# Kernel tuning notes

Hardware: AMD Instinct MI355X
Metric: run time of the kernel (lower is better)

The kernel has to match this reference:

```python
import jax, jax.numpy as jnp
import numpy as np

B, MAX_T, S, H, NB, NA = 64, 511, 1024, 4096, 8, 4


def setup_inputs() -> dict:
    key = jax.random.key(0)
    k1, k2, k3, k4, k5 = jax.random.split(key, 5)
    s_i_batch = jax.random.normal(k1, (B, MAX_T + 1, S), dtype=jnp.float32)
    actions_batch = jax.random.randint(k2, (B, MAX_T), 0, NA, dtype=jnp.int32)
    lengths = jax.random.randint(k3, (B,), 0, MAX_T, dtype=jnp.int32)
    W1 = jax.random.normal(k4, (S, H), dtype=jnp.float32) * (1.0 / np.sqrt(S))
    b1 = jnp.zeros((H,), dtype=jnp.float32)
    W2 = jax.random.normal(k5, (H, NB * NA), dtype=jnp.float32) * (1.0 / np.sqrt(H))
    b2 = jnp.zeros((NB * NA,), dtype=jnp.float32)
    return {"s_i_batch": s_i_batch, "actions_batch": actions_batch,
            "lengths": lengths, "W1": W1, "b1": b1, "W2": W2, "b2": b2}


def reference(s_i_batch, actions_batch, lengths, W1, b1, W2, b2):
    Bc, Tp1, _ = s_i_batch.shape
    maxT = Tp1 - 1
    # control_net: MLP -> per-(option, action) log-probs
    h = jax.nn.relu(jnp.einsum('bts,sh->bth', s_i_batch, W1) + b1)
    logits = (jnp.einsum('bth,ha->bta', h, W2) + b2).reshape(Bc, Tp1, NB, NA)
    action_logps = jax.nn.log_softmax(logits, axis=-1)  # (B, T+1, b, 4)
    # option 0, timesteps 0..max_T-1
    lp0 = action_logps[:, :maxT, 0, :]                  # (B, max_T, 4)
    gathered = jnp.take_along_axis(lp0, actions_batch[..., None].astype(jnp.int32), axis=-1)[..., 0]
    mask = (jnp.arange(maxT)[None, :] < lengths[:, None]).astype(lp0.dtype)  # (B, max_T)
    total_logp = jnp.sum(gathered * mask)
    return -total_logp
```

## Files before the change

kernel.cpp:

```cpp
#include <hip/hip_runtime.h>
#include <hip/hip_bf16.h>
#include <math.h>

#define B_    64
#define MAXT  511
#define TP1   512
#define S_    1024
#define H_    4096
#define M_TOTAL (B_*TP1)
#define NITER (S_/32)

typedef __attribute__((ext_vector_type(8))) short  short8;
typedef __attribute__((ext_vector_type(4))) float  float4v;

#define ZBUF_BYTES (M_TOTAL*4*sizeof(float))
#define ACC_OFF    ZBUF_BYTES
#define SBF_OFF    0x81000
#define SBF_BYTES  ((size_t)M_TOTAL*S_*2)
#define W1T_OFF    (SBF_OFF + SBF_BYTES)

static __device__ __forceinline__ unsigned short f2bf(float f) {
    unsigned int u = __float_as_uint(f);
    u = u + 0x7fffu + ((u >> 16) & 1u);
    return (unsigned short)(u >> 16);
}

__global__ __launch_bounds__(128) void cvt_s_kernel(const float* __restrict__ s,
                                                    const int* __restrict__ lengths,
                                                    unsigned short* __restrict__ out) {
    int row = blockIdx.x;
    int b = row >> 9, t = row & 511;
    if (t >= lengths[b]) return;
    size_t idx = (size_t)row * S_ + threadIdx.x * 8;
    float4v f0 = *(const float4v*)(s + idx);
    float4v f1 = *(const float4v*)(s + idx + 4);
    short8 o;
    o[0] = (short)f2bf(f0[0]); o[1] = (short)f2bf(f0[1]);
    o[2] = (short)f2bf(f0[2]); o[3] = (short)f2bf(f0[3]);
    o[4] = (short)f2bf(f1[0]); o[5] = (short)f2bf(f1[1]);
    o[6] = (short)f2bf(f1[2]); o[7] = (short)f2bf(f1[3]);
    *(short8*)(out + idx) = o;
}

__global__ void cvt_w1t_kernel(const float* __restrict__ W1, unsigned short* __restrict__ W1T) {
    __shared__ float tile[32][33];
    int h0 = blockIdx.x * 32;
    int k0 = blockIdx.y * 32;
    int tx = threadIdx.x & 31, ty = threadIdx.x >> 5;
    for (int r = ty; r < 32; r += 8)
        tile[r][tx] = W1[(size_t)(k0 + r) * H_ + h0 + tx];
    __syncthreads();
    for (int r = ty; r < 32; r += 8)
        W1T[(size_t)(h0 + r) * S_ + k0 + tx] = f2bf(tile[tx][r]);
}

__global__ __launch_bounds__(256) void gemm_fused_kernel(
        const unsigned short* __restrict__ Sb,
        const unsigned short* __restrict__ W1T,
        const float* __restrict__ b1,
        const float* __restrict__ W2,
        const int*   __restrict__ lengths,
        float*       __restrict__ zbuf)
{
    int ntile = blockIdx.x;
    int mtile = blockIdx.y;
    int b  = mtile >> 2;
    int t0 = (mtile & 3) * 128;
    if (lengths[b] <= t0) return;

    int m0 = mtile * 128;
    int n0 = ntile * 128;

    __shared__ unsigned short smemA[2 * 128 * 32];
    __shared__ unsigned short smemB[2 * 128 * 32];

    int tid  = threadIdx.x;
    int wid  = tid >> 6;
    int lane = tid & 63;
    int lane15 = lane & 15;
    int quad   = lane >> 4;
    int wave_m = (wid >> 1) * 64;
    int wave_n = (wid & 1) * 64;

    int cA0 = tid, cA1 = tid + 256;
    int mA0 = cA0 >> 2, cp0 = cA0 & 3, q0 = cp0 ^ ((mA0 >> 1) & 3);
    int mA1 = cA1 >> 2, cp1 = cA1 & 3, q1 = cp1 ^ ((mA1 >> 1) & 3);

    const char* gA0 = (const char*)Sb  + (size_t)(m0 + mA0) * (S_*2) + q0 * 16;
    const char* gA1 = (const char*)Sb  + (size_t)(m0 + mA1) * (S_*2) + q1 * 16;
    const char* gB0 = (const char*)W1T + (size_t)(n0 + mA0) * (S_*2) + q0 * 16;
    const char* gB1 = (const char*)W1T + (size_t)(n0 + mA1) * (S_*2) + q1 * 16;
    char* lwA0 = (char*)smemA + cA0 * 16;
    char* lwA1 = (char*)smemA + cA1 * 16;
    char* lwB0 = (char*)smemB + cA0 * 16;
    char* lwB1 = (char*)smemB + cA1 * 16;

    int aOff[4], bOff[4];
#pragma unroll
    for (int s = 0; s < 4; s++) {
        int ml = wave_m + s * 16 + lane15;
        aOff[s] = ml * 32 + (quad ^ ((ml >> 1) & 3)) * 8;
        int nl = wave_n + s * 16 + lane15;
        bOff[s] = nl * 32 + (quad ^ ((nl >> 1) & 3)) * 8;
    }

    float4v acc[4][4] = {};
    short8 rA0[2], rA1[2], rB0[2], rB1[2];

    rA0[0] = *(const short8*)gA0; rA1[0] = *(const short8*)gA1;
    rB0[0] = *(const short8*)gB0; rB1[0] = *(const short8*)gB1;
    gA0 += 64; gA1 += 64; gB0 += 64; gB1 += 64;
    *(short8*)lwA0 = rA0[0]; *(short8*)lwA1 = rA1[0];
    *(short8*)lwB0 = rB0[0]; *(short8*)lwB1 = rB1[0];
    rA0[1] = *(const short8*)gA0; rA1[1] = *(const short8*)gA1;
    rB0[1] = *(const short8*)gB0; rB1[1] = *(const short8*)gB1;
    gA0 += 64; gA1 += 64; gB0 += 64; gB1 += 64;

    for (int k = 0; k < NITER; k += 2) {
        __syncthreads();
        if (k + 2 < NITER) {
            rA0[0] = *(const short8*)gA0; rA1[0] = *(const short8*)gA1;
            rB0[0] = *(const short8*)gB0; rB1[0] = *(const short8*)gB1;
            gA0 += 64; gA1 += 64; gB0 += 64; gB1 += 64;
        }
        *(short8*)(lwA0 + 8192) = rA0[1]; *(short8*)(lwA1 + 8192) = rA1[1];
        *(short8*)(lwB0 + 8192) = rB0[1]; *(short8*)(lwB1 + 8192) = rB1[1];
        {
            const unsigned short* aP = smemA;
            const unsigned short* bP = smemB;
            short8 af[4], bf[4];
#pragma unroll
            for (int s = 0; s < 4; s++) {
                af[s] = *(const short8*)(aP + aOff[s]);
                bf[s] = *(const short8*)(bP + bOff[s]);
            }
#pragma unroll
            for (int i = 0; i < 4; i++)
#pragma unroll
                for (int j = 0; j < 4; j++)
                    acc[i][j] = __builtin_amdgcn_mfma_f32_16x16x32_bf16(af[i], bf[j], acc[i][j], 0, 0, 0);
        }
        __syncthreads();
        if (k + 3 < NITER) {
            rA0[1] = *(const short8*)gA0; rA1[1] = *(const short8*)gA1;
            rB0[1] = *(const short8*)gB0; rB1[1] = *(const short8*)gB1;
            gA0 += 64; gA1 += 64; gB0 += 64; gB1 += 64;
        }
        if (k + 2 < NITER) {
            *(short8*)lwA0 = rA0[0]; *(short8*)lwA1 = rA1[0];
            *(short8*)lwB0 = rB0[0]; *(short8*)lwB1 = rB1[0];
        }
        {
            const unsigned short* aP = smemA + 4096;
            const unsigned short* bP = smemB + 4096;
            short8 af[4], bf[4];
#pragma unroll
            for (int s = 0; s < 4; s++) {
                af[s] = *(const short8*)(aP + aOff[s]);
                bf[s] = *(const short8*)(bP + bOff[s]);
            }
#pragma unroll
            for (int i = 0; i < 4; i++)
#pragma unroll
                for (int j = 0; j < 4; j++)
                    acc[i][j] = __builtin_amdgcn_mfma_f32_16x16x32_bf16(af[i], bf[j], acc[i][j], 0, 0, 0);
        }
    }

    float4v w2r[4];
    float   b1v[4];
#pragma unroll
    for (int ns = 0; ns < 4; ns++) {
        int n_g = n0 + wave_n + ns * 16 + lane15;
        w2r[ns] = *(const float4v*)(W2 + (size_t)n_g * 32);
        b1v[ns] = b1[n_g];
    }
#pragma unroll
    for (int ms = 0; ms < 4; ms++) {
        float p[4][4];
#pragma unroll
        for (int r = 0; r < 4; r++)
#pragma unroll
            for (int c = 0; c < 4; c++) p[r][c] = 0.f;
#pragma unroll
        for (int ns = 0; ns < 4; ns++) {
            float4v av = acc[ms][ns];
#pragma unroll
            for (int r = 0; r < 4; r++) {
                float h = av[r] + b1v[ns];
                h = h > 0.f ? h : 0.f;
                p[r][0] += h * w2r[ns][0];
                p[r][1] += h * w2r[ns][1];
                p[r][2] += h * w2r[ns][2];
                p[r][3] += h * w2r[ns][3];
            }
        }
#pragma unroll
        for (int off = 1; off < 16; off <<= 1)
#pragma unroll
            for (int r = 0; r < 4; r++)
#pragma unroll
                for (int c = 0; c < 4; c++)
                    p[r][c] += __shfl_xor(p[r][c], off);
        if (lane15 < 4) {
            int c = lane15;
#pragma unroll
            for (int r = 0; r < 4; r++) {
                int mg = m0 + wave_m + ms * 16 + quad * 4 + r;
                atomicAdd(&zbuf[(size_t)mg * 4 + c], p[r][c]);
            }
        }
    }
}

__global__ __launch_bounds__(128) void reduce_logp_kernel(
        const float* __restrict__ zbuf,
        const int*   __restrict__ actions,
        const int*   __restrict__ lengths,
        const float* __restrict__ b2,
        float*       __restrict__ acc)
{
    int b = blockIdx.x;
    int t = blockIdx.y * 128 + threadIdx.x;
    int len = lengths[b];
    float local = 0.f;
    if (t < MAXT && t < len) {
        int row = b * TP1 + t;
        float4v z = *(const float4v*)(zbuf + (size_t)row * 4);
        float z0 = z[0] + b2[0], z1 = z[1] + b2[1], z2 = z[2] + b2[2], z3 = z[3] + b2[3];
        float mx = fmaxf(fmaxf(z0, z1), fmaxf(z2, z3));
        float se = expf(z0 - mx) + expf(z1 - mx) + expf(z2 - mx) + expf(z3 - mx);
        int a = actions[b * MAXT + t];
        float za = (a == 0) ? z0 : (a == 1) ? z1 : (a == 2) ? z2 : z3;
        local += (za - mx) - logf(se);
    }
#pragma unroll
    for (int off = 32; off > 0; off >>= 1) local += __shfl_xor(local, off);
    __shared__ float wsum[2];
    if ((threadIdx.x & 63) == 0) wsum[threadIdx.x >> 6] = local;
    __syncthreads();
    if (threadIdx.x == 0) atomicAdd(acc, wsum[0] + wsum[1]);
}

__global__ void finalize_kernel(const float* __restrict__ acc, float* __restrict__ out) {
    out[0] = -acc[0];
}

extern "C" void kernel_launch(void* const* d_in, const int* in_sizes, int n_in,
                              void* d_out, int out_size, void* d_ws, size_t ws_size,
                              hipStream_t stream) {
    const float* s       = (const float*)d_in[0];
    const int*   actions = (const int*)  d_in[1];
    const int*   lengths = (const int*)  d_in[2];
    const float* W1      = (const float*)d_in[3];
    const float* b1      = (const float*)d_in[4];
    const float* W2      = (const float*)d_in[5];
    const float* b2      = (const float*)d_in[6];

    char* ws = (char*)d_ws;
    float*          zbuf = (float*)ws;
    float*          acc  = (float*)(ws + ACC_OFF);
    unsigned short* Sb   = (unsigned short*)(ws + SBF_OFF);
    unsigned short* W1T  = (unsigned short*)(ws + W1T_OFF);

    hipMemsetAsync(ws, 0, ZBUF_BYTES + 256, stream);

    cvt_s_kernel<<<dim3(M_TOTAL), 128, 0, stream>>>(s, lengths, Sb);
    cvt_w1t_kernel<<<dim3(H_ / 32, S_ / 32), 256, 0, stream>>>(W1, W1T);
    gemm_fused_kernel<<<dim3(H_ / 128, M_TOTAL / 128), 256, 0, stream>>>(
        Sb, W1T, b1, W2, lengths, zbuf);
    reduce_logp_kernel<<<dim3(B_, 4), 128, 0, stream>>>(zbuf, actions, lengths, b2, acc);
    finalize_kernel<<<dim3(1), 1, 0, stream>>>(acc, (float*)d_out);
}
```

Before: 529.7 us.

## Merge conversion kernels, remap GEMM tiles per XCD, drop finalize kernel

Folds the two bf16 conversion kernels into one prep kernel that uses nontemporal loads, and removes the finalize kernel by having the reduction atomically accumulate the negated sum straight into the output. The GEMM grid becomes 1D and is remapped so that each of the 8 XCDs works on a contiguous group of 4 N-tiles, so the W1T columns it reads stay in that XCD's L2. The aim is fewer launches and better cache locality for W1T. The cost is an extra memset for the output and a tile order that assumes round-robin dispatch of blocks across XCDs.

```diff
diff --git a/kernel.cpp b/kernel.cpp
--- a/kernel.cpp
+++ b/kernel.cpp
@@ -13,8 +13,7 @@
 typedef __attribute__((ext_vector_type(8))) short  short8;
 typedef __attribute__((ext_vector_type(4))) float  float4v;
 
-#define ZBUF_BYTES (M_TOTAL*4*sizeof(float))
-#define ACC_OFF    ZBUF_BYTES
+#define ZBUF_BYTES ((size_t)M_TOTAL*4*sizeof(float))
 #define SBF_OFF    0x81000
 #define SBF_BYTES  ((size_t)M_TOTAL*S_*2)
 #define W1T_OFF    (SBF_OFF + SBF_BYTES)
@@ -25,33 +24,37 @@
     return (unsigned short)(u >> 16);
 }
 
-__global__ __launch_bounds__(128) void cvt_s_kernel(const float* __restrict__ s,
-                                                    const int* __restrict__ lengths,
-                                                    unsigned short* __restrict__ out) {
-    int row = blockIdx.x;
-    int b = row >> 9, t = row & 511;
-    if (t >= lengths[b]) return;
-    size_t idx = (size_t)row * S_ + threadIdx.x * 8;
-    float4v f0 = *(const float4v*)(s + idx);
-    float4v f1 = *(const float4v*)(s + idx + 4);
-    short8 o;
-    o[0] = (short)f2bf(f0[0]); o[1] = (short)f2bf(f0[1]);
-    o[2] = (short)f2bf(f0[2]); o[3] = (short)f2bf(f0[3]);
-    o[4] = (short)f2bf(f1[0]); o[5] = (short)f2bf(f1[1]);
-    o[6] = (short)f2bf(f1[2]); o[7] = (short)f2bf(f1[3]);
-    *(short8*)(out + idx) = o;
-}
-
-__global__ void cvt_w1t_kernel(const float* __restrict__ W1, unsigned short* __restrict__ W1T) {
-    __shared__ float tile[32][33];
-    int h0 = blockIdx.x * 32;
-    int k0 = blockIdx.y * 32;
-    int tx = threadIdx.x & 31, ty = threadIdx.x >> 5;
-    for (int r = ty; r < 32; r += 8)
-        tile[r][tx] = W1[(size_t)(k0 + r) * H_ + h0 + tx];
-    __syncthreads();
-    for (int r = ty; r < 32; r += 8)
-        W1T[(size_t)(h0 + r) * S_ + k0 + tx] = f2bf(tile[tx][r]);
+__global__ __launch_bounds__(256) void prep_kernel(const float* __restrict__ s,
+                                                   const float* __restrict__ W1,
+                                                   const int*   __restrict__ lengths,
+                                                   unsigned short* __restrict__ Sb,
+                                                   unsigned short* __restrict__ W1T) {
+    int bid = blockIdx.x;
+    if (bid < 16384) {
+        int row = 2 * bid + (threadIdx.x >> 7);
+        int b = row >> 9, t = row & 511;
+        if (t >= lengths[b]) return;
+        size_t idx = (size_t)row * S_ + (threadIdx.x & 127) * 8;
+        float4v f0 = __builtin_nontemporal_load((const float4v*)(s + idx));
+        float4v f1 = __builtin_nontemporal_load((const float4v*)(s + idx + 4));
+        short8 o;
+        o[0] = (short)f2bf(f0[0]); o[1] = (short)f2bf(f0[1]);
+        o[2] = (short)f2bf(f0[2]); o[3] = (short)f2bf(f0[3]);
+        o[4] = (short)f2bf(f1[0]); o[5] = (short)f2bf(f1[1]);
+        o[6] = (short)f2bf(f1[2]); o[7] = (short)f2bf(f1[3]);
+        *(short8*)(Sb + idx) = o;
+    } else {
+        __shared__ float tile[32][33];
+        int tb = bid - 16384;
+        int h0 = (tb & 127) * 32;
+        int k0 = (tb >> 7) * 32;
+        int tx = threadIdx.x & 31, ty = threadIdx.x >> 5;
+        for (int r = ty; r < 32; r += 8)
+            tile[r][tx] = __builtin_nontemporal_load(&W1[(size_t)(k0 + r) * H_ + h0 + tx]);
+        __syncthreads();
+        for (int r = ty; r < 32; r += 8)
+            W1T[(size_t)(h0 + r) * S_ + k0 + tx] = f2bf(tile[tx][r]);
+    }
 }
 
 __global__ __launch_bounds__(256) void gemm_fused_kernel(
@@ -62,8 +65,12 @@
         const int*   __restrict__ lengths,
         float*       __restrict__ zbuf)
 {
-    int ntile = blockIdx.x;
-    int mtile = blockIdx.y;
+    int id   = blockIdx.x;
+    int xcd  = id & 7;
+    int slot = id >> 3;
+    int ntile = xcd * 4 + (slot & 3);
+    int mtile = slot >> 2;
+
     int b  = mtile >> 2;
     int t0 = (mtile & 3) * 128;
     if (lengths[b] <= t0) return;
@@ -218,7 +225,7 @@
         const int*   __restrict__ actions,
         const int*   __restrict__ lengths,
         const float* __restrict__ b2,
-        float*       __restrict__ acc)
+        float*       __restrict__ out)
 {
     int b = blockIdx.x;
     int t = blockIdx.y * 128 + threadIdx.x;
@@ -232,18 +239,14 @@
         float se = expf(z0 - mx) + expf(z1 - mx) + expf(z2 - mx) + expf(z3 - mx);
         int a = actions[b * MAXT + t];
         float za = (a == 0) ? z0 : (a == 1) ? z1 : (a == 2) ? z2 : z3;
-        local += (za - mx) - logf(se);
+        local = (za - mx) - logf(se);
     }
 #pragma unroll
     for (int off = 32; off > 0; off >>= 1) local += __shfl_xor(local, off);
     __shared__ float wsum[2];
     if ((threadIdx.x & 63) == 0) wsum[threadIdx.x >> 6] = local;
     __syncthreads();
-    if (threadIdx.x == 0) atomicAdd(acc, wsum[0] + wsum[1]);
-}
-
-__global__ void finalize_kernel(const float* __restrict__ acc, float* __restrict__ out) {
-    out[0] = -acc[0];
+    if (threadIdx.x == 0) atomicAdd(out, -(wsum[0] + wsum[1]));
 }
 
 extern "C" void kernel_launch(void* const* d_in, const int* in_sizes, int n_in,
@@ -259,16 +262,13 @@
 
     char* ws = (char*)d_ws;
     float*          zbuf = (float*)ws;
-    float*          acc  = (float*)(ws + ACC_OFF);
     unsigned short* Sb   = (unsigned short*)(ws + SBF_OFF);
     unsigned short* W1T  = (unsigned short*)(ws + W1T_OFF);
 
-    hipMemsetAsync(ws, 0, ZBUF_BYTES + 256, stream);
-
-    cvt_s_kernel<<<dim3(M_TOTAL), 128, 0, stream>>>(s, lengths, Sb);
-    cvt_w1t_kernel<<<dim3(H_ / 32, S_ / 32), 256, 0, stream>>>(W1, W1T);
-    gemm_fused_kernel<<<dim3(H_ / 128, M_TOTAL / 128), 256, 0, stream>>>(
-        Sb, W1T, b1, W2, lengths, zbuf);
-    reduce_logp_kernel<<<dim3(B_, 4), 128, 0, stream>>>(zbuf, actions, lengths, b2, acc);
-    finalize_kernel<<<dim3(1), 1, 0, stream>>>(acc, (float*)d_out);
-}
+    hipMemsetAsync(ws, 0, ZBUF_BYTES, stream);
+    hipMemsetAsync(d_out, 0, sizeof(float), stream);
+
+    prep_kernel<<<dim3(16384 + 4096), 256, 0, stream>>>(s, W1, lengths, Sb, W1T);
+    gemm_fused_kernel<<<dim3(8192), 256, 0, stream>>>(Sb, W1T, b1, W2, lengths, zbuf);
+    reduce_logp_kernel<<<dim3(B_, 4), 128, 0, stream>>>(zbuf, actions, lengths, b2, (float*)d_out);
+}
```

Result: no change. 525.6 us (-0.8%).
